# Performance work log

Measured on AMD Instinct MI355X. Metric: run time of the kernel, lower is better.

Reference implementation:

```python
import jax, jax.numpy as jnp
import numpy as np

N = 50000
E = 1600000
F_IN = 256
HEADS = 4
HID = 32
C = 16
NEG_SLOPE = 0.2


def _add_self_loops(edge_index, n):
    loop = jnp.arange(n, dtype=edge_index.dtype)
    return jnp.concatenate([edge_index, jnp.stack([loop, loop])], axis=1)


def gat_conv(x, edge_index, W, att_src, att_dst, bias, heads, n):
    # PyG GATConv (concat=True, add_self_loops=True, inference: no dropout)
    ei = _add_self_loops(edge_index, n)
    src, dst = ei[0], ei[1]
    d = W.shape[1] // heads
    xw = (x @ W).reshape(n, heads, d)                      # [N,H,D]
    a_src = jnp.sum(xw * att_src, axis=-1)                 # [N,H]
    a_dst = jnp.sum(xw * att_dst, axis=-1)                 # [N,H]
    e = jax.nn.leaky_relu(a_src[src] + a_dst[dst], NEG_SLOPE)  # [E',H]
    # segment softmax over destination neighborhoods
    m = jax.ops.segment_max(e, dst, num_segments=n)        # [N,H]
    ex = jnp.exp(e - m[dst])
    denom = jax.ops.segment_sum(ex, dst, num_segments=n)   # [N,H]
    alpha = ex / denom[dst]                                # [E',H]
    msg = xw[src] * alpha[:, :, None]                      # [E',H,D]
    out = jax.ops.segment_sum(msg, dst, num_segments=n)    # [N,H,D]
    return out.reshape(n, heads * d) + bias


def setup_inputs() -> dict:
    key = jax.random.key(0)
    ks = jax.random.split(key, 10)
    g = lambda k, shape, fan: jax.random.normal(k, shape, jnp.float32) * (1.0 / np.sqrt(fan))
    x = jax.random.normal(ks[0], (N, F_IN), jnp.float32)
    edge_index = jax.random.randint(ks[1], (2, E), 0, N, dtype=jnp.int64)
    return {
        "x": x,
        "edge_index": edge_index,
        "W1": g(ks[2], (F_IN, HEADS * HID), F_IN),
        "att_src1": g(ks[3], (HEADS, HID), HID),
        "att_dst1": g(ks[4], (HEADS, HID), HID),
        "b1": jnp.zeros((HEADS * HID,), jnp.float32),
        "W2": g(ks[5], (HEADS * HID, C), HEADS * HID),
        "att_src2": g(ks[6], (1, C), C),
        "att_dst2": g(ks[7], (1, C), C),
        "b2": jnp.zeros((C,), jnp.float32),
    }


def reference(x, edge_index, W1, att_src1, att_dst1, b1, W2, att_src2, att_dst2, b2):
    h = gat_conv(x, edge_index, W1, att_src1, att_dst1, b1, HEADS, N)
    h = jax.nn.relu(h)
    # dropout: identity at inference (training=False)
    out = gat_conv(h, edge_index, W2, att_src2, att_dst2, b2, 1, N)
    return jax.nn.log_softmax(out, axis=1)
```

## Files before the change

kernel.cpp:

```cpp
#include <hip/hip_runtime.h>
#include <hip/hip_bf16.h>

typedef __hip_bfloat16 bf16;
typedef long long i64;
typedef unsigned long long u64;
typedef __attribute__((ext_vector_type(8))) short short8;
typedef __attribute__((ext_vector_type(4))) float floatx4;

#define NN    50000
#define EE    1600000
#define E2    1650000
#define FIN   256
#define HD    128
#define NH    4
#define NC    16
#define SLOPE 0.2f
#define K     128
#define DPB   391
#define CAPB  16384
#define CAP   15360
#define CH2   2048

#define KS_S  2312

#define OF_FLAGS 0
#define OF_BCUR  16
#define OF_BBASE 144
#define OF_RP    280
#define OF_W1T   50284
#define OF_BIN   66668
#define OF_CSR   4260972
#define OF_XQ    5910972
#define OF_SC    7510972
#define OF_AS1   7610972
#define OF_AD1   7810972
#define OF_HW2   8010972
#define OF_AS2   8810972
#define OF_AD2   8860972

__device__ __forceinline__ float b2f(bf16 v) { return __bfloat162float(v); }
__device__ __forceinline__ float us2f(unsigned short u) {
    return __uint_as_float(((unsigned)u) << 16);
}
__device__ __forceinline__ unsigned short f2us(float f) {
    unsigned u = __float_as_uint(f);
    return (unsigned short)((u + 0x7fffu + ((u >> 16) & 1u)) >> 16);
}
__device__ __forceinline__ float lrelu(float v) { return v > 0.f ? v : SLOPE * v; }
__device__ __forceinline__ float ub2f(unsigned u, int sh) {
    return (float)((u >> sh) & 0xffu);
}
__device__ __forceinline__ int fwi(int node, int ch) {
    return node * 132 + (ch >> 5) * 33 + (ch & 31);
}

template <bool F32>
__device__ __forceinline__ float ldin(const void* p, int i) {
    if (F32) return ((const float*)p)[i];
    return b2f(((const bf16*)p)[i]);
}
template <bool F32>
__device__ __forceinline__ float4 ldin4(const void* p, int i) {
    if (F32) return *(const float4*)((const float*)p + i);
    ushort4 u = *(const ushort4*)((const unsigned short*)p + i);
    float4 r;
    r.x = us2f(u.x); r.y = us2f(u.y); r.z = us2f(u.z); r.w = us2f(u.w);
    return r;
}

__device__ __forceinline__ void edge_sd(const void* ei, int f64, int e, int& s, int& d) {
    if (e >= EE) { s = e - EE; d = s; return; }
    if (f64) {
        s = (int)((const i64*)ei)[e];
        d = (int)((const i64*)ei)[EE + e];
    } else {
        s = ((const int*)ei)[e];
        d = ((const int*)ei)[EE + e];
    }
    s = min(max(s, 0), NN - 1);
    d = min(max(d, 0), NN - 1);
}

__global__ void detect(const void* x, const void* ei, int* flags, int* bcur) {
    __shared__ int cnt[2];
    int t = threadIdx.x;
    if (t < K) bcur[t] = t * CAPB;
    if (t == 0) { cnt[0] = 0; cnt[1] = 0; }
    __syncthreads();
    const unsigned short* xb = (const unsigned short*)x;
    int c0 = 0;
    for (int i = t; i < 4096; i += 256) {
        float v = __uint_as_float(((unsigned)xb[2 * i]) << 16);
        if (!(fabsf(v) < 1e6f)) c0++;
    }
    const i64* e64 = (const i64*)ei;
    int c1 = 0;
    for (int i = t; i < 1024; i += 256) {
        i64 v = e64[i];
        if (v >= 0 && v < NN) c1++;
    }
    atomicAdd(&cnt[0], c0);
    atomicAdd(&cnt[1], c1);
    __syncthreads();
    if (t == 0) {
        flags[0] = (cnt[0] > 400) ? 1 : 0;
        flags[1] = (cnt[1] >= 1000) ? 1 : 0;
    }
}

template <bool F32>
__global__ void trW(const void* __restrict__ W1, const int* __restrict__ flags,
                    unsigned short* __restrict__ w1t) {
    if (flags[0] != (F32 ? 1 : 0)) return;
    int t = blockIdx.x * 256 + threadIdx.x;
    int k = t >> 5, n4 = (t & 31) * 4;
    float4 v = ldin4<F32>(W1, k * HD + n4);
    int ks = k >> 5, kk = k & 31;
    w1t[((ks * HD + n4 + 0) * 32) + kk] = f2us(v.x);
    w1t[((ks * HD + n4 + 1) * 32) + kk] = f2us(v.y);
    w1t[((ks * HD + n4 + 2) * 32) + kk] = f2us(v.z);
    w1t[((ks * HD + n4 + 3) * 32) + kk] = f2us(v.w);
}

__global__ __launch_bounds__(256) void binScatter(const void* __restrict__ ei,
                                                  const int* __restrict__ flags,
                                                  int* __restrict__ bcur,
                                                  u64* __restrict__ bin) {
    __shared__ int h[K], res[K];
    int t = threadIdx.x;
    int base = blockIdx.x * CH2 + t * 8;
    if (t < K) h[t] = 0;
    __syncthreads();
    int f64 = flags[1];
    int sv[8], dv[8], rk[8];
    int n_ = 0;
    if (!f64 && base + 8 <= EE) {
        const int* es = (const int*)ei;
        int4 a = *(const int4*)&es[base];
        int4 b = *(const int4*)&es[base + 4];
        int4 c = *(const int4*)&es[EE + base];
        int4 g = *(const int4*)&es[EE + base + 4];
        sv[0] = a.x; sv[1] = a.y; sv[2] = a.z; sv[3] = a.w;
        sv[4] = b.x; sv[5] = b.y; sv[6] = b.z; sv[7] = b.w;
        dv[0] = c.x; dv[1] = c.y; dv[2] = c.z; dv[3] = c.w;
        dv[4] = g.x; dv[5] = g.y; dv[6] = g.z; dv[7] = g.w;
#pragma unroll
        for (int i = 0; i < 8; i++) {
            sv[i] = min(max(sv[i], 0), NN - 1);
            dv[i] = min(max(dv[i], 0), NN - 1);
        }
        n_ = 8;
    } else {
        for (int i = 0; i < 8; i++) {
            int e = base + i;
            if (e < E2) {
                int s, d; edge_sd(ei, f64, e, s, d);
                sv[n_] = s; dv[n_] = d; n_++;
            }
        }
    }
#pragma unroll 8
    for (int i = 0; i < n_; i++) rk[i] = atomicAdd(&h[dv[i] / DPB], 1);
    __syncthreads();
    if (t < K) res[t] = h[t] ? atomicAdd(&bcur[t], h[t]) : 0;
    __syncthreads();
#pragma unroll 8
    for (int i = 0; i < n_; i++) {
        int b = dv[i] / DPB;
        int pos = res[b] + rk[i];
        pos = min(pos, (b + 1) * CAPB - 1);
        bin[pos] = (((u64)(unsigned)dv[i]) << 32) | (unsigned)sv[i];
    }
}

__global__ void bucketScan(const int* __restrict__ bcur, int* __restrict__ bbase) {
    __shared__ int sh[K];
    int t = threadIdx.x;
    int v = min(bcur[t] - t * CAPB, CAPB);
    sh[t] = v;
    __syncthreads();
    for (int off = 1; off < K; off <<= 1) {
        int u = (t >= off) ? sh[t - off] : 0;
        __syncthreads();
        sh[t] += u;
        __syncthreads();
    }
    bbase[t] = sh[t] - v;
    if (t == K - 1) bbase[K] = sh[K - 1];
}

__global__ __launch_bounds__(256) void csrB(const u64* __restrict__ bin,
                                            const int* __restrict__ bbase,
                                            int* __restrict__ rp, int* __restrict__ csr) {
    __shared__ int cnt[512];
    __shared__ int cur[DPB];
    __shared__ int buf[CAP];
    int b = blockIdx.x, t = threadIdx.x;
    int d0 = b * DPB;
    int nd = min(DPB, NN - d0);
    int src0 = b * CAPB;
    int base = bbase[b], size = bbase[b + 1] - base;
    cnt[t] = 0; cnt[t + 256] = 0;
    __syncthreads();
    for (int i = t; i < size; i += 256) {
        int d = (int)(bin[src0 + i] >> 32);
        atomicAdd(&cnt[d - d0], 1);
    }
    __syncthreads();
    int a0 = cnt[2 * t], a1 = cnt[2 * t + 1];
    int ps = a0 + a1;
    buf[t] = ps;
    __syncthreads();
    for (int off = 1; off < 256; off <<= 1) {
        int u = (t >= off) ? buf[t - off] : 0;
        __syncthreads();
        buf[t] += u;
        __syncthreads();
    }
    int ex = buf[t] - ps;
    __syncthreads();
    cnt[2 * t] = ex;
    cnt[2 * t + 1] = ex + a0;
    __syncthreads();
    for (int i = t; i < nd; i += 256) {
        rp[d0 + i] = base + cnt[i];
        cur[i] = cnt[i];
    }
    if (b == K - 1 && t == 0) rp[NN] = bbase[K];
    __syncthreads();
    if (size <= CAP) {
        for (int i = t; i < size; i += 256) {
            u64 p = bin[src0 + i];
            int pos = atomicAdd(&cur[(int)(p >> 32) - d0], 1);
            buf[pos] = (int)(unsigned)p;
        }
        __syncthreads();
        for (int i = t; i < size; i += 256) csr[base + i] = buf[i];
    } else {
        for (int i = t; i < size; i += 256) {
            u64 p = bin[src0 + i];
            int pos = base + atomicAdd(&cur[(int)(p >> 32) - d0], 1);
            csr[pos] = (int)(unsigned)p;
        }
    }
}

template <bool F32>
__global__ __launch_bounds__(256) void gemm1(
    const void* __restrict__ x, const unsigned short* __restrict__ w1t,
    const void* __restrict__ as1, const void* __restrict__ ad1,
    const int* __restrict__ flags, signed char* __restrict__ xq, float* __restrict__ sc2,
    float* __restrict__ asrc, float* __restrict__ adst) {
    if (flags[0] != (F32 ? 1 : 0)) return;
    __shared__ unsigned short af[8 * KS_S];
    __shared__ float scl[128];
    int t = threadIdx.x;
    int m0 = blockIdx.x * 64;
#pragma unroll
    for (int i = 0; i < 16; i++) {
        int slot = i * 256 + t;
        int mi = slot >> 6, k4 = (slot & 63) * 4;
        float4 v = make_float4(0.f, 0.f, 0.f, 0.f);
        if (m0 + mi < NN) v = ldin4<F32>(x, (m0 + mi) * FIN + k4);
        ushort4 o;
        o.x = f2us(v.x); o.y = f2us(v.y); o.z = f2us(v.z); o.w = f2us(v.w);
        *(ushort4*)&af[(k4 >> 5) * KS_S + mi * 36 + (k4 & 31)] = o;
    }
    __syncthreads();
    int w = t >> 6, lane = t & 63;
    int col = lane & 15, q = lane >> 4;
    floatx4 acc[4][2];
#pragma unroll
    for (int mt = 0; mt < 4; mt++)
#pragma unroll
        for (int u = 0; u < 2; u++) { acc[mt][u].x = 0.f; acc[mt][u].y = 0.f; acc[mt][u].z = 0.f; acc[mt][u].w = 0.f; }
#pragma unroll
    for (int ks = 0; ks < 8; ks++) {
        short8 bf0 = *(const short8*)&w1t[(ks * HD + w * 32 + col) * 32 + q * 8];
        short8 bf1 = *(const short8*)&w1t[(ks * HD + w * 32 + 16 + col) * 32 + q * 8];
#pragma unroll
        for (int mt = 0; mt < 4; mt++) {
            short8 afr = *(const short8*)&af[ks * KS_S + (mt * 16 + col) * 36 + q * 8];
            acc[mt][0] = __builtin_amdgcn_mfma_f32_16x16x32_bf16(afr, bf0, acc[mt][0], 0, 0, 0);
            acc[mt][1] = __builtin_amdgcn_mfma_f32_16x16x32_bf16(afr, bf1, acc[mt][1], 0, 0, 0);
        }
    }
    __syncthreads();
    float* fw = (float*)af;
#pragma unroll
    for (int mt = 0; mt < 4; mt++)
#pragma unroll
        for (int u = 0; u < 2; u++)
#pragma unroll
            for (int r = 0; r < 4; r++) {
                int node = mt * 16 + q * 4 + r;
                fw[fwi(node, w * 32 + u * 16 + col)] = acc[mt][u][r];
            }
    __syncthreads();
    int node = t >> 2, part = t & 3;
    {
        float amax = 0.f;
#pragma unroll
        for (int c = 0; c < 32; c++) amax = fmaxf(amax, fabsf(fw[fwi(node, part * 32 + c)]));
        amax = fmaxf(amax, __shfl_xor(amax, 1));
        if ((part & 1) == 0) {
            scl[node * 2 + (part >> 1)] = (amax > 0.f) ? 127.f / amax : 0.f;
            if (m0 + node < NN) sc2[(m0 + node) * 2 + (part >> 1)] = amax * (1.f / 127.f);
        }
    }
    __syncthreads();
    if (m0 + node < NN) {
        float inv = scl[node * 2 + (part >> 1)];
        unsigned dw[8];
#pragma unroll
        for (int g = 0; g < 8; g++) {
            unsigned pk = 0;
#pragma unroll
            for (int j = 0; j < 4; j++) {
                float v = fw[fwi(node, part * 32 + g * 4 + j)];
                int qi = (int)rintf(v * inv);
                qi = min(127, max(-127, qi));
                pk |= ((unsigned)((qi + 128) & 255)) << (8 * j);
            }
            dw[g] = pk;
        }
        *(uint4*)&xq[(m0 + node) * HD + part * 32]      = make_uint4(dw[0], dw[1], dw[2], dw[3]);
        *(uint4*)&xq[(m0 + node) * HD + part * 32 + 16] = make_uint4(dw[4], dw[5], dw[6], dw[7]);
        float s = 0.f, dd = 0.f;
#pragma unroll
        for (int c = 0; c < 32; c++) {
            float xv = fw[fwi(node, part * 32 + c)];
            s  += xv * ldin<F32>(as1, part * 32 + c);
            dd += xv * ldin<F32>(ad1, part * 32 + c);
        }
        asrc[(m0 + node) * NH + part] = s;
        adst[(m0 + node) * NH + part] = dd;
    }
}

template <bool F32>
__global__ __launch_bounds__(128) void node1(
    const int* __restrict__ rp, const int* __restrict__ cs,
    const float* __restrict__ asrc, const float* __restrict__ adst,
    const signed char* __restrict__ xq, const float* __restrict__ sc2,
    const void* __restrict__ b1, const void* __restrict__ W2,
    const void* __restrict__ as2, const void* __restrict__ ad2,
    const int* __restrict__ flags, float* __restrict__ hw2,
    float* __restrict__ asrc2, float* __restrict__ adst2) {
    if (flags[0] != (F32 ? 1 : 0)) return;
    int d = blockIdx.x, t = threadIdx.x;
    int beg = rp[d], end = rp[d + 1];
    int deg = end - beg;
    __shared__ float sw[64][4];
    __shared__ int   ss[64];
    __shared__ float red[2][HD];
    __shared__ float wv[2][4];
    __shared__ float hs[HD];
    __shared__ float l2[32];
    int hw_ = t & 3;
    float adw = adst[d * NH + hw_];
    int cg = t & 15, eo = t >> 4, head = cg >> 2;
    float acc[8];
#pragma unroll
    for (int j = 0; j < 8; j++) acc[j] = 0.f;
    float wacc = 0.f, wss = 0.f;
    const unsigned* xqu = (const unsigned*)xq;
    int sl = t >> 2;
    int m = min(deg, 64);
    int nIt = (m + 7) >> 3;
    int ec0 = beg + sl, ec1 = beg + sl + 32;
    int s0 = cs[min(ec0, E2 - 1)];
    int s1 = cs[min(ec1, E2 - 1)];
    int sg[8];
#pragma unroll
    for (int k = 0; k < 8; k++)
        if (k < nIt) sg[k] = cs[min(beg + eo + 8 * k, E2 - 1)];
    float a0 = asrc[s0 * NH + hw_];
    float a1 = asrc[s1 * NH + hw_];
    float q0 = sc2[s0 * 2 + (hw_ >> 1)];
    float q1 = sc2[s1 * 2 + (hw_ >> 1)];
    uint2 uv[8];
#pragma unroll
    for (int k = 0; k < 8; k++)
        if (k < nIt) uv[k] = *(const uint2*)&xqu[sg[k] * 32 + cg * 2];
    float w0 = 0.f, c0 = 0.f, w1 = 0.f, c1 = 0.f;
    if (ec0 < end) { w0 = __expf(fminf(lrelu(a0 + adw), 80.f)); c0 = w0 * q0; }
    if (ec1 < end) { w1 = __expf(fminf(lrelu(a1 + adw), 80.f)); c1 = w1 * q1; }
    sw[sl][hw_] = c0;
    sw[sl + 32][hw_] = c1;
    wacc = w0 + w1;
    __syncthreads();
#pragma unroll
    for (int k = 0; k < 8; k++)
        if (k < nIt) {
            float we = sw[eo + 8 * k][head];
            uint2 u = uv[k];
            acc[0] += we * ub2f(u.x, 0);
            acc[1] += we * ub2f(u.x, 8);
            acc[2] += we * ub2f(u.x, 16);
            acc[3] += we * ub2f(u.x, 24);
            acc[4] += we * ub2f(u.y, 0);
            acc[5] += we * ub2f(u.y, 8);
            acc[6] += we * ub2f(u.y, 16);
            acc[7] += we * ub2f(u.y, 24);
            wss += we;
        }
    for (int chb = beg + 64; chb < end; chb += 32) {
        __syncthreads();
        int ec = chb + sl;
        float w = 0.f, wsc = 0.f;
        int s = 0;
        if (ec < end) {
            s = cs[ec];
            w = __expf(fminf(lrelu(asrc[s * NH + hw_] + adw), 80.f));
            wsc = w * sc2[s * 2 + (hw_ >> 1)];
        }
        sw[sl][hw_] = wsc;
        if (hw_ == 0) ss[sl] = s;
        wacc += w;
        __syncthreads();
        int mm = min(32, end - chb);
        for (int e = eo; e < mm; e += 8) {
            float we = sw[e][head];
            int s2 = ss[e];
            uint2 u = *(const uint2*)&xqu[s2 * 32 + cg * 2];
            acc[0] += we * ub2f(u.x, 0);
            acc[1] += we * ub2f(u.x, 8);
            acc[2] += we * ub2f(u.x, 16);
            acc[3] += we * ub2f(u.x, 24);
            acc[4] += we * ub2f(u.y, 0);
            acc[5] += we * ub2f(u.y, 8);
            acc[6] += we * ub2f(u.y, 16);
            acc[7] += we * ub2f(u.y, 24);
            wss += we;
        }
    }
#pragma unroll
    for (int j = 0; j < 8; j++) acc[j] -= 128.f * wss;
    wacc += __shfl_xor(wacc, 4);
    wacc += __shfl_xor(wacc, 8);
    wacc += __shfl_xor(wacc, 16);
    wacc += __shfl_xor(wacc, 32);
    int wid = t >> 6, lane = t & 63;
    if (lane < 4) wv[wid][lane] = wacc;
#pragma unroll
    for (int j = 0; j < 8; j++) {
        acc[j] += __shfl_xor(acc[j], 16);
        acc[j] += __shfl_xor(acc[j], 32);
    }
    if (lane < 16) {
#pragma unroll
        for (int j = 0; j < 8; j++) red[wid][lane * 8 + j] = acc[j];
    }
    __syncthreads();
    float tot = red[0][t] + red[1][t];
    float wt  = wv[0][t >> 5] + wv[1][t >> 5];
    hs[t] = fmaxf(tot / wt + ldin<F32>(b1, t), 0.f);
    __syncthreads();
    int j = t & 15, g = t >> 4;
    float p = 0.f;
#pragma unroll
    for (int k = 0; k < 16; k++) p += hs[g * 16 + k] * ldin<F32>(W2, (g * 16 + k) * NC + j);
    p += __shfl_xor(p, 16);
    p += __shfl_xor(p, 32);
    if ((t & 63) < 16) l2[(t >> 6) * 16 + j] = p;
    __syncthreads();
    if (t < 16) {
        float hw = l2[t] + l2[16 + t];
        hw2[d * NC + t] = hw;
        float a2s = hw * ldin<F32>(as2, t);
        float a2d = hw * ldin<F32>(ad2, t);
#pragma unroll
        for (int off = 8; off; off >>= 1) {
            a2s += __shfl_xor(a2s, off, 16);
            a2d += __shfl_xor(a2d, off, 16);
        }
        if (t == 0) { asrc2[d] = a2s; adst2[d] = a2d; }
    }
}

template <bool F32>
__global__ __launch_bounds__(256) void node2(
    const int* __restrict__ rp, const int* __restrict__ cs,
    const float* __restrict__ asrc2, const float* __restrict__ adst2,
    const float* __restrict__ hw2, const void* __restrict__ b2,
    const int* __restrict__ flags, void* __restrict__ out) {
    if (flags[0] != (F32 ? 1 : 0)) return;
    int t = threadIdx.x, wid = t >> 6, lane = t & 63;
    int d = blockIdx.x * 4 + wid;
    if (d >= NN) return;
    int beg = rp[d], end = rp[d + 1];
    float ad = adst2[d];
    int q = lane & 3, eo = lane >> 2;
    float4 acc = make_float4(0.f, 0.f, 0.f, 0.f);
    float wtot = 0.f;
    for (int chb = beg; chb < end; chb += 64) {
        int ec = chb + lane;
        float w = 0.f;
        int s = 0;
        if (ec < end) {
            s = cs[ec];
            w = __expf(fminf(lrelu(asrc2[s] + ad), 80.f));
        }
        float ws = w;
        ws += __shfl_xor(ws, 1);
        ws += __shfl_xor(ws, 2);
        ws += __shfl_xor(ws, 4);
        ws += __shfl_xor(ws, 8);
        ws += __shfl_xor(ws, 16);
        ws += __shfl_xor(ws, 32);
        wtot += ws;
        int mm = min(64, end - chb);
        int nk = (mm + 15) >> 4;
#pragma unroll
        for (int k = 0; k < 4; k++)
            if (k < nk) {
                int e = eo + k * 16;
                float we = __shfl(w, e);
                int s2 = __shfl(s, e);
                float4 v = *(const float4*)&hw2[s2 * NC + q * 4];
                acc.x += we * v.x; acc.y += we * v.y;
                acc.z += we * v.z; acc.w += we * v.w;
            }
    }
#pragma unroll
    for (int off = 4; off < 64; off <<= 1) {
        acc.x += __shfl_xor(acc.x, off);
        acc.y += __shfl_xor(acc.y, off);
        acc.z += __shfl_xor(acc.z, off);
        acc.w += __shfl_xor(acc.w, off);
    }
    float rw = 1.f / wtot;
    float v0 = acc.x * rw + ldin<F32>(b2, q * 4 + 0);
    float v1 = acc.y * rw + ldin<F32>(b2, q * 4 + 1);
    float v2 = acc.z * rw + ldin<F32>(b2, q * 4 + 2);
    float v3 = acc.w * rw + ldin<F32>(b2, q * 4 + 3);
    float mx = fmaxf(fmaxf(v0, v1), fmaxf(v2, v3));
    mx = fmaxf(mx, __shfl_xor(mx, 1));
    mx = fmaxf(mx, __shfl_xor(mx, 2));
    float es = __expf(v0 - mx) + __expf(v1 - mx) + __expf(v2 - mx) + __expf(v3 - mx);
    es += __shfl_xor(es, 1);
    es += __shfl_xor(es, 2);
    float lse = mx + __logf(es);
    if (lane < 4) {
        if (F32) {
            *(float4*)&((float*)out)[d * NC + q * 4] =
                make_float4(v0 - lse, v1 - lse, v2 - lse, v3 - lse);
        } else {
            bf16* o = (bf16*)out + d * NC + q * 4;
            o[0] = __float2bfloat16(v0 - lse); o[1] = __float2bfloat16(v1 - lse);
            o[2] = __float2bfloat16(v2 - lse); o[3] = __float2bfloat16(v3 - lse);
        }
    }
}

extern "C" void kernel_launch(void* const* d_in, const int* in_sizes, int n_in,
                              void* d_out, int out_size, void* d_ws, size_t ws_size,
                              hipStream_t stream) {
    const void* x   = d_in[0];
    const void* ei  = d_in[1];
    const void* W1  = d_in[2];
    const void* as1 = d_in[3];
    const void* ad1 = d_in[4];
    const void* b1  = d_in[5];
    const void* W2  = d_in[6];
    const void* as2 = d_in[7];
    const void* ad2 = d_in[8];
    const void* b2v = d_in[9];

    float* ws = (float*)d_ws;
    int* flags = (int*)(ws + OF_FLAGS);
    int* bcur  = (int*)(ws + OF_BCUR);
    int* bbase = (int*)(ws + OF_BBASE);
    int* rp    = (int*)(ws + OF_RP);
    unsigned short* w1t = (unsigned short*)(ws + OF_W1T);
    u64* bin   = (u64*)(ws + OF_BIN);
    int* csr   = (int*)(ws + OF_CSR);
    signed char* xq = (signed char*)(ws + OF_XQ);
    float* sc2   = ws + OF_SC;
    float* asrc1 = ws + OF_AS1;
    float* adst1 = ws + OF_AD1;
    float* hw2   = ws + OF_HW2;
    float* asrc2 = ws + OF_AS2;
    float* adst2 = ws + OF_AD2;

    detect<<<1, 256, 0, stream>>>(x, ei, flags, bcur);
    trW<true><<<32, 256, 0, stream>>>(W1, flags, w1t);
    binScatter<<<(E2 + CH2 - 1) / CH2, 256, 0, stream>>>(ei, flags, bcur, bin);
    bucketScan<<<1, K, 0, stream>>>(bcur, bbase);
    csrB<<<K, 256, 0, stream>>>(bin, bbase, rp, csr);

    const int GB = (NN + 63) / 64;
    gemm1<true><<<GB, 256, 0, stream>>>(x, w1t, as1, ad1, flags, xq, sc2, asrc1, adst1);
    node1<true><<<NN, 128, 0, stream>>>(rp, csr, asrc1, adst1, xq, sc2, b1, W2, as2, ad2,
                                        flags, hw2, asrc2, adst2);
    node2<true><<<(NN + 3) / 4, 256, 0, stream>>>(rp, csr, asrc2, adst2, hw2, b2v, flags,
                                                  d_out);
}
```

Before: 295.8 us.

## Fuse edge binning into GEMM launch, merge bucket scan into CSR build

The edge bin-scatter is merged into the layer-1 GEMM kernel as extra blocks, so edge binning runs concurrently with the dense projection in one launch. The bucket prefix scan is folded into every CSR-build block, and the bucket count doubles from 128 to 256 with smaller per-bucket capacity, giving more CSR blocks. node2 now issues its hw2 gathers before the exp and reduction so the loads overlap. This removes two launches and idle time but uses more shared memory in the fused kernel, and the smaller per-bucket capacity raises overflow risk for skewed degrees.

```diff
diff --git a/kernel.cpp b/kernel.cpp
--- a/kernel.cpp
+++ b/kernel.cpp
@@ -15,28 +15,30 @@
 #define NH    4
 #define NC    16
 #define SLOPE 0.2f
-#define K     128
-#define DPB   391
-#define CAPB  16384
-#define CAP   15360
+#define KB    256
+#define DPB   196
+#define CAPB  8960
+#define CAP   8960
 #define CH2   2048
+#define GBC   782
+#define EBC   806
 
 #define KS_S  2312
 
 #define OF_FLAGS 0
 #define OF_BCUR  16
-#define OF_BBASE 144
-#define OF_RP    280
-#define OF_W1T   50284
-#define OF_BIN   66668
-#define OF_CSR   4260972
-#define OF_XQ    5910972
-#define OF_SC    7510972
-#define OF_AS1   7610972
-#define OF_AD1   7810972
-#define OF_HW2   8010972
-#define OF_AS2   8810972
-#define OF_AD2   8860972
+#define OF_BBASE 272
+#define OF_RP    544
+#define OF_W1T   50548
+#define OF_BIN   66932
+#define OF_CSR   4654452
+#define OF_XQ    6304452
+#define OF_SC    7904452
+#define OF_AS1   8004452
+#define OF_AD1   8204452
+#define OF_HW2   8404452
+#define OF_AS2   9204452
+#define OF_AD2   9254452
 
 __device__ __forceinline__ float b2f(bf16 v) { return __bfloat162float(v); }
 __device__ __forceinline__ float us2f(unsigned short u) {
@@ -84,7 +86,7 @@
 __global__ void detect(const void* x, const void* ei, int* flags, int* bcur) {
     __shared__ int cnt[2];
     int t = threadIdx.x;
-    if (t < K) bcur[t] = t * CAPB;
+    if (t < KB) bcur[t] = t * CAPB;
     if (t == 0) { cnt[0] = 0; cnt[1] = 0; }
     __syncthreads();
     const unsigned short* xb = (const unsigned short*)x;
@@ -122,139 +124,67 @@
     w1t[((ks * HD + n4 + 3) * 32) + kk] = f2us(v.w);
 }
 
-__global__ __launch_bounds__(256) void binScatter(const void* __restrict__ ei,
-                                                  const int* __restrict__ flags,
-                                                  int* __restrict__ bcur,
-                                                  u64* __restrict__ bin) {
-    __shared__ int h[K], res[K];
-    int t = threadIdx.x;
-    int base = blockIdx.x * CH2 + t * 8;
-    if (t < K) h[t] = 0;
-    __syncthreads();
-    int f64 = flags[1];
-    int sv[8], dv[8], rk[8];
-    int n_ = 0;
-    if (!f64 && base + 8 <= EE) {
-        const int* es = (const int*)ei;
-        int4 a = *(const int4*)&es[base];
-        int4 b = *(const int4*)&es[base + 4];
-        int4 c = *(const int4*)&es[EE + base];
-        int4 g = *(const int4*)&es[EE + base + 4];
-        sv[0] = a.x; sv[1] = a.y; sv[2] = a.z; sv[3] = a.w;
-        sv[4] = b.x; sv[5] = b.y; sv[6] = b.z; sv[7] = b.w;
-        dv[0] = c.x; dv[1] = c.y; dv[2] = c.z; dv[3] = c.w;
-        dv[4] = g.x; dv[5] = g.y; dv[6] = g.z; dv[7] = g.w;
-#pragma unroll
-        for (int i = 0; i < 8; i++) {
-            sv[i] = min(max(sv[i], 0), NN - 1);
-            dv[i] = min(max(dv[i], 0), NN - 1);
-        }
-        n_ = 8;
-    } else {
-        for (int i = 0; i < 8; i++) {
-            int e = base + i;
-            if (e < E2) {
-                int s, d; edge_sd(ei, f64, e, s, d);
-                sv[n_] = s; dv[n_] = d; n_++;
-            }
-        }
-    }
-#pragma unroll 8
-    for (int i = 0; i < n_; i++) rk[i] = atomicAdd(&h[dv[i] / DPB], 1);
-    __syncthreads();
-    if (t < K) res[t] = h[t] ? atomicAdd(&bcur[t], h[t]) : 0;
-    __syncthreads();
-#pragma unroll 8
-    for (int i = 0; i < n_; i++) {
-        int b = dv[i] / DPB;
-        int pos = res[b] + rk[i];
-        pos = min(pos, (b + 1) * CAPB - 1);
-        bin[pos] = (((u64)(unsigned)dv[i]) << 32) | (unsigned)sv[i];
-    }
-}
-
-__global__ void bucketScan(const int* __restrict__ bcur, int* __restrict__ bbase) {
-    __shared__ int sh[K];
-    int t = threadIdx.x;
-    int v = min(bcur[t] - t * CAPB, CAPB);
-    sh[t] = v;
-    __syncthreads();
-    for (int off = 1; off < K; off <<= 1) {
-        int u = (t >= off) ? sh[t - off] : 0;
-        __syncthreads();
-        sh[t] += u;
-        __syncthreads();
-    }
-    bbase[t] = sh[t] - v;
-    if (t == K - 1) bbase[K] = sh[K - 1];
-}
-
-__global__ __launch_bounds__(256) void csrB(const u64* __restrict__ bin,
-                                            const int* __restrict__ bbase,
-                                            int* __restrict__ rp, int* __restrict__ csr) {
-    __shared__ int cnt[512];
-    __shared__ int cur[DPB];
-    __shared__ int buf[CAP];
-    int b = blockIdx.x, t = threadIdx.x;
-    int d0 = b * DPB;
-    int nd = min(DPB, NN - d0);
-    int src0 = b * CAPB;
-    int base = bbase[b], size = bbase[b + 1] - base;
-    cnt[t] = 0; cnt[t + 256] = 0;
-    __syncthreads();
-    for (int i = t; i < size; i += 256) {
-        int d = (int)(bin[src0 + i] >> 32);
-        atomicAdd(&cnt[d - d0], 1);
-    }
-    __syncthreads();
-    int a0 = cnt[2 * t], a1 = cnt[2 * t + 1];
-    int ps = a0 + a1;
-    buf[t] = ps;
-    __syncthreads();
-    for (int off = 1; off < 256; off <<= 1) {
-        int u = (t >= off) ? buf[t - off] : 0;
-        __syncthreads();
-        buf[t] += u;
-        __syncthreads();
-    }
-    int ex = buf[t] - ps;
-    __syncthreads();
-    cnt[2 * t] = ex;
-    cnt[2 * t + 1] = ex + a0;
-    __syncthreads();
-    for (int i = t; i < nd; i += 256) {
-        rp[d0 + i] = base + cnt[i];
-        cur[i] = cnt[i];
-    }
-    if (b == K - 1 && t == 0) rp[NN] = bbase[K];
-    __syncthreads();
-    if (size <= CAP) {
-        for (int i = t; i < size; i += 256) {
-            u64 p = bin[src0 + i];
-            int pos = atomicAdd(&cur[(int)(p >> 32) - d0], 1);
-            buf[pos] = (int)(unsigned)p;
-        }
-        __syncthreads();
-        for (int i = t; i < size; i += 256) csr[base + i] = buf[i];
-    } else {
-        for (int i = t; i < size; i += 256) {
-            u64 p = bin[src0 + i];
-            int pos = base + atomicAdd(&cur[(int)(p >> 32) - d0], 1);
-            csr[pos] = (int)(unsigned)p;
-        }
-    }
-}
-
 template <bool F32>
-__global__ __launch_bounds__(256) void gemm1(
+__global__ __launch_bounds__(256) void gsFuse(
     const void* __restrict__ x, const unsigned short* __restrict__ w1t,
     const void* __restrict__ as1, const void* __restrict__ ad1,
-    const int* __restrict__ flags, signed char* __restrict__ xq, float* __restrict__ sc2,
-    float* __restrict__ asrc, float* __restrict__ adst) {
-    if (flags[0] != (F32 ? 1 : 0)) return;
+    const void* __restrict__ ei, const int* __restrict__ flags,
+    signed char* __restrict__ xq, float* __restrict__ sc2,
+    float* __restrict__ asrc, float* __restrict__ adst,
+    int* __restrict__ bcur, u64* __restrict__ bin) {
     __shared__ unsigned short af[8 * KS_S];
     __shared__ float scl[128];
+    __shared__ int hh[KB], res[KB];
     int t = threadIdx.x;
+
+    if (blockIdx.x >= GBC) {
+        int base = (blockIdx.x - GBC) * CH2 + t * 8;
+        if (t < KB) hh[t] = 0;
+        __syncthreads();
+        int f64 = flags[1];
+        int sv[8], dv[8], rk[8];
+        int n_ = 0;
+        if (!f64 && base + 8 <= EE) {
+            const int* es = (const int*)ei;
+            int4 a = *(const int4*)&es[base];
+            int4 b = *(const int4*)&es[base + 4];
+            int4 c = *(const int4*)&es[EE + base];
+            int4 g = *(const int4*)&es[EE + base + 4];
+            sv[0] = a.x; sv[1] = a.y; sv[2] = a.z; sv[3] = a.w;
+            sv[4] = b.x; sv[5] = b.y; sv[6] = b.z; sv[7] = b.w;
+            dv[0] = c.x; dv[1] = c.y; dv[2] = c.z; dv[3] = c.w;
+            dv[4] = g.x; dv[5] = g.y; dv[6] = g.z; dv[7] = g.w;
+#pragma unroll
+            for (int i = 0; i < 8; i++) {
+                sv[i] = min(max(sv[i], 0), NN - 1);
+                dv[i] = min(max(dv[i], 0), NN - 1);
+            }
+            n_ = 8;
+        } else {
+            for (int i = 0; i < 8; i++) {
+                int e = base + i;
+                if (e < E2) {
+                    int s, d; edge_sd(ei, f64, e, s, d);
+                    sv[n_] = s; dv[n_] = d; n_++;
+                }
+            }
+        }
+#pragma unroll 8
+        for (int i = 0; i < n_; i++) rk[i] = atomicAdd(&hh[dv[i] / DPB], 1);
+        __syncthreads();
+        if (t < KB) res[t] = hh[t] ? atomicAdd(&bcur[t], hh[t]) : 0;
+        __syncthreads();
+#pragma unroll 8
+        for (int i = 0; i < n_; i++) {
+            int b = dv[i] / DPB;
+            int pos = res[b] + rk[i];
+            pos = min(pos, (b + 1) * CAPB - 1);
+            bin[pos] = (((u64)(unsigned)dv[i]) << 32) | (unsigned)sv[i];
+        }
+        return;
+    }
+
+    if (flags[0] != (F32 ? 1 : 0)) return;
     int m0 = blockIdx.x * 64;
 #pragma unroll
     for (int i = 0; i < 16; i++) {
@@ -335,6 +265,72 @@
         }
         asrc[(m0 + node) * NH + part] = s;
         adst[(m0 + node) * NH + part] = dd;
+    }
+}
+
+__global__ __launch_bounds__(256) void csrB(const int* __restrict__ bcur,
+                                            const u64* __restrict__ bin,
+                                            int* __restrict__ rp, int* __restrict__ csr) {
+    __shared__ int cnt[512];
+    __shared__ int cur[DPB];
+    __shared__ int buf[CAP];
+    __shared__ int sc[KB];
+    int b = blockIdx.x, t = threadIdx.x;
+    sc[t] = min(bcur[t] - t * CAPB, CAPB);
+    __syncthreads();
+    for (int off = 1; off < KB; off <<= 1) {
+        int u = (t >= off) ? sc[t - off] : 0;
+        __syncthreads();
+        sc[t] += u;
+        __syncthreads();
+    }
+    int base = b ? sc[b - 1] : 0;
+    int size = sc[b] - base;
+    if (b == KB - 1 && t == 0) rp[NN] = sc[KB - 1];
+    int d0 = b * DPB;
+    int nd = min(DPB, NN - d0);
+    int src0 = b * CAPB;
+    cnt[t] = 0; cnt[t + 256] = 0;
+    __syncthreads();
+    for (int i = t; i < size; i += 256) {
+        int d = (int)(bin[src0 + i] >> 32);
+        atomicAdd(&cnt[d - d0], 1);
+    }
+    __syncthreads();
+    int a0 = cnt[2 * t], a1 = cnt[2 * t + 1];
+    int ps = a0 + a1;
+    buf[t] = ps;
+    __syncthreads();
+    for (int off = 1; off < 256; off <<= 1) {
+        int u = (t >= off) ? buf[t - off] : 0;
+        __syncthreads();
+        buf[t] += u;
+        __syncthreads();
+    }
+    int ex = buf[t] - ps;
+    __syncthreads();
+    cnt[2 * t] = ex;
+    cnt[2 * t + 1] = ex + a0;
+    __syncthreads();
+    for (int i = t; i < nd; i += 256) {
+        rp[d0 + i] = base + cnt[i];
+        cur[i] = cnt[i];
+    }
+    __syncthreads();
+    if (size <= CAP) {
+        for (int i = t; i < size; i += 256) {
+            u64 p = bin[src0 + i];
+            int pos = atomicAdd(&cur[(int)(p >> 32) - d0], 1);
+            buf[pos] = (int)(unsigned)p;
+        }
+        __syncthreads();
+        for (int i = t; i < size; i += 256) csr[base + i] = buf[i];
+    } else {
+        for (int i = t; i < size; i += 256) {
+            u64 p = bin[src0 + i];
+            int pos = base + atomicAdd(&cur[(int)(p >> 32) - d0], 1);
+            csr[pos] = (int)(unsigned)p;
+        }
     }
 }
 
@@ -496,12 +492,21 @@
     float wtot = 0.f;
     for (int chb = beg; chb < end; chb += 64) {
         int ec = chb + lane;
+        int s = 0;
+        bool val = ec < end;
+        if (val) s = cs[ec];
+        int mm = min(64, end - chb);
+        int nk = (mm + 15) >> 4;
+        float4 v[4];
+        int s2a[4];
+#pragma unroll
+        for (int k = 0; k < 4; k++)
+            if (k < nk) s2a[k] = __shfl(s, eo + k * 16);
+#pragma unroll
+        for (int k = 0; k < 4; k++)
+            if (k < nk) v[k] = *(const float4*)&hw2[s2a[k] * NC + q * 4];
         float w = 0.f;
-        int s = 0;
-        if (ec < end) {
-            s = cs[ec];
-            w = __expf(fminf(lrelu(asrc2[s] + ad), 80.f));
-        }
+        if (val) w = __expf(fminf(lrelu(asrc2[s] + ad), 80.f));
         float ws = w;
         ws += __shfl_xor(ws, 1);
         ws += __shfl_xor(ws, 2);
@@ -510,17 +515,12 @@
         ws += __shfl_xor(ws, 16);
         ws += __shfl_xor(ws, 32);
         wtot += ws;
-        int mm = min(64, end - chb);
-        int nk = (mm + 15) >> 4;
 #pragma unroll
         for (int k = 0; k < 4; k++)
             if (k < nk) {
-                int e = eo + k * 16;
-                float we = __shfl(w, e);
-                int s2 = __shfl(s, e);
-                float4 v = *(const float4*)&hw2[s2 * NC + q * 4];
-                acc.x += we * v.x; acc.y += we * v.y;
-                acc.z += we * v.z; acc.w += we * v.w;
+                float we = __shfl(w, eo + k * 16);
+                acc.x += we * v[k].x; acc.y += we * v[k].y;
+                acc.z += we * v[k].z; acc.w += we * v[k].w;
             }
     }
 #pragma unroll
@@ -571,7 +571,6 @@
     float* ws = (float*)d_ws;
     int* flags = (int*)(ws + OF_FLAGS);
     int* bcur  = (int*)(ws + OF_BCUR);
-    int* bbase = (int*)(ws + OF_BBASE);
     int* rp    = (int*)(ws + OF_RP);
     unsigned short* w1t = (unsigned short*)(ws + OF_W1T);
     u64* bin   = (u64*)(ws + OF_BIN);
@@ -586,12 +585,9 @@
 
     detect<<<1, 256, 0, stream>>>(x, ei, flags, bcur);
     trW<true><<<32, 256, 0, stream>>>(W1, flags, w1t);
-    binScatter<<<(E2 + CH2 - 1) / CH2, 256, 0, stream>>>(ei, flags, bcur, bin);
-    bucketScan<<<1, K, 0, stream>>>(bcur, bbase);
-    csrB<<<K, 256, 0, stream>>>(bin, bbase, rp, csr);
-
-    const int GB = (NN + 63) / 64;
-    gemm1<true><<<GB, 256, 0, stream>>>(x, w1t, as1, ad1, flags, xq, sc2, asrc1, adst1);
+    gsFuse<true><<<GBC + EBC, 256, 0, stream>>>(x, w1t, as1, ad1, ei, flags, xq, sc2,
+                                                asrc1, adst1, bcur, bin);
+    csrB<<<KB, 256, 0, stream>>>(bcur, bin, rp, csr);
     node1<true><<<NN, 128, 0, stream>>>(rp, csr, asrc1, adst1, xq, sc2, b1, W2, as2, ad2,
                                         flags, hw2, asrc2, adst2);
     node2<true><<<(NN + 3) / 4, 256, 0, stream>>>(rp, csr, asrc2, adst2, hw2, b2v, flags,
```

New measurement: 270.9 us. -8.4%, faster.
